# Kernel tuning notes

Hardware: AMD Instinct MI355X
Metric: run time of the kernel (lower is better)

Reference implementation:

```python
import jax, jax.numpy as jnp
import numpy as np

B, S, D, C = 4, 4096, 2048, 64  # batch, seq, d_model, num_channels (sqrt(4096)=64)
TEMP = 1.0
LN_EPS = 1e-5
AGG_EPS = 1e-8


def _layer_norm(x, g, b):
    m = x.mean(-1, keepdims=True)
    v = ((x - m) ** 2).mean(-1, keepdims=True)
    return (x - m) / jnp.sqrt(v + LN_EPS) * g + b


def setup_inputs() -> dict:
    key = jax.random.key(0)
    ks = jax.random.split(key, 8)
    s = 1.0 / np.sqrt(D)
    return {
        "x": jax.random.normal(ks[0], (B, S, D), jnp.float32),
        "attention_mask": jnp.ones((B, S), jnp.float32),
        "ln_gamma": jnp.ones((D,), jnp.float32),
        "ln_beta": jnp.zeros((D,), jnp.float32),
        "Wq": jax.random.normal(ks[1], (D, D), jnp.float32) * s,
        "Wk": jax.random.normal(ks[2], (D, D), jnp.float32) * s,
        "Wv": jax.random.normal(ks[3], (D, D), jnp.float32) * s,
        "Wr": jax.random.normal(ks[4], (C, D), jnp.float32) * s,
        "br": jnp.zeros((C,), jnp.float32),
        "Wa": jax.random.normal(ks[5], (D, D), jnp.float32) * s,
        "ba": jnp.zeros((D,), jnp.float32),
        "Wout": jax.random.normal(ks[6], (D, D), jnp.float32) * s,
        "bout": jnp.zeros((D,), jnp.float32),
    }


def reference(x, attention_mask, ln_gamma, ln_beta, Wq, Wk, Wv, Wr, br, Wa, ba, Wout, bout):
    residual = x
    h = _layer_norm(x, ln_gamma, ln_beta)
    q = h @ Wq.T  # [B,S,D]
    k = h @ Wk.T
    v = h @ Wv.T
    m = attention_mask[..., None]
    q = q * m
    k = k * m
    v = v * m

    # --- dynamic router: logits -> softmax, top-1 channel id + gathered weight ---
    routing_input = q + 0.1 * k
    probs = jax.nn.softmax((routing_input @ Wr.T + br) / TEMP, axis=-1)  # [B,S,C]
    channel_ids = jnp.argmax(probs, axis=-1)  # [B,S] int
    w = jnp.take_along_axis(probs, channel_ids[..., None], axis=-1)  # [B,S,1] top-1 weight

    # --- learnable channel aggregator: scatter-reduce tokens -> channels ---
    onehot = jax.nn.one_hot(channel_ids, C, dtype=v.dtype)  # [B,S,C]
    dispatch = onehot * w  # weighted dispatch mask
    ch_sum = jnp.einsum('bsc,bsd->bcd', dispatch, v)  # [B,C,D]
    ch_den = dispatch.sum(axis=1)  # [B,C]
    ch_mean = ch_sum / (ch_den[..., None] + AGG_EPS)
    ch_out = ch_mean @ Wa.T + ba  # learnable channel transform [B,C,D]
    # gather channel summary back to each token, weighted by routing weight
    aggregated = jnp.einsum('bsc,bcd->bsd', onehot, ch_out) * w  # [B,S,D]

    # --- regularization term ---
    q_norm = jnp.linalg.norm(q, axis=-1, keepdims=True)
    k_norm = jnp.linalg.norm(k, axis=-1, keepdims=True)
    reg = 0.001 * (q_norm + k_norm).mean()

    output = aggregated @ Wout.T + bout
    output = output + reg  # broadcast scalar reg_term
    output = output + residual
    return output
```

## Files before the change

kernel.cpp:

```cpp
#include <hip/hip_runtime.h>
#include <hip/hip_bf16.h>

typedef unsigned short u16;
typedef __bf16 bf16x8 __attribute__((ext_vector_type(8)));
typedef float  f32x4  __attribute__((ext_vector_type(4)));

#define B_   4
#define S_   4096
#define D_   2048
#define C_   64
#define T_   (B_*S_)
#define NALL 6144
#define NCH  16

__device__ __forceinline__ u16 f2bf(float f) {
  union { float f; unsigned u; } c; c.f = f;
  unsigned r = c.u + 0x7FFFu + ((c.u >> 16) & 1u);
  return (u16)(r >> 16);
}
__device__ __forceinline__ float bf2f(u16 u) {
  union { float f; unsigned u; } c; c.u = ((unsigned)u) << 16;
  return c.f;
}

__device__ __forceinline__ void gload16(const u16* g, u16* l) {
  __builtin_amdgcn_global_load_lds(
      (__attribute__((address_space(1))) void*)(void*)g,
      (__attribute__((address_space(3))) void*)l, 16, 0, 0);
}

#define BAR()  { __builtin_amdgcn_s_barrier(); __builtin_amdgcn_sched_barrier(0); }
#define VMW(N) { asm volatile("s_waitcnt vmcnt(" #N ")" ::: "memory"); __builtin_amdgcn_sched_barrier(0); }

template<int REGB, int TYPE>
__device__ __forceinline__ void stage_ht(const u16* __restrict__ Mat, char* lds,
                                         int bufbyte, int kelem, int wid, int lane)
{
#pragma unroll
  for (int j = 0; j < 2; ++j) {
    int sr;
    if (TYPE == 0)      sr = (j ?  64 :   0) + wid * 8;
    else if (TYPE == 1) sr = (j ? 192 : 128) + wid * 8;
    else if (TYPE == 2) sr = (j ? 128 :   0) + wid * 8;
    else                sr = (j ? 192 :  64) + wid * 8;
    int r  = sr + (lane >> 3);
    int kc = (lane & 7) ^ (lane >> 3);
    const u16* src = Mat + (size_t)r * 2048 + kelem + kc * 8;
    u16* dst = (u16*)(lds + bufbyte + REGB * 32768 + sr * 128 + lane * 16);
    gload16(src, dst);
  }
}

__global__ __launch_bounds__(512, 2)
void qkv8(const u16* __restrict__ A, const u16* __restrict__ BT,
          const float* __restrict__ mask,
          float* __restrict__ qn2, float* __restrict__ kn2,
          u16* __restrict__ vout)
{
  extern __shared__ char lds[];
  const int tid = threadIdx.x;
  const int wid = tid >> 6, lane = tid & 63;
  const int wm = wid >> 2, wn = wid & 3;
  const int lcol = lane & 15, lhi = lane >> 4, lc7 = lane & 7;
  const int bm = blockIdx.x, bn = blockIdx.y;

  const u16* Ab_ = A  + (size_t)bm * 256 * 2048;
  const u16* Bb_ = BT + (size_t)bn * 256 * 2048;

  f32x4 acc[8][4] = {};
  bf16x8 afr[4][2], bfr[4][2];

#define LDA_(f_, s_) (*(const bf16x8*)(lds + cbyte + ((wm*128 + (f_)*16 + lcol) * 128) + (((lhi + (s_)*4) ^ lc7) << 4)))
#define LDB_(g_, s_) (*(const bf16x8*)(lds + cbyte + 32768 + ((wn*64 + (g_)*16 + lcol) * 128) + (((lhi + (s_)*4) ^ lc7) << 4)))

  stage_ht<1, 0>(Bb_, lds, 0, 0, wid, lane);
  stage_ht<1, 1>(Bb_, lds, 0, 0, wid, lane);
  stage_ht<0, 2>(Ab_, lds, 0, 0, wid, lane);
  stage_ht<0, 3>(Ab_, lds, 0, 0, wid, lane);
  VMW(2); BAR();

#pragma unroll 2
  for (int kt = 0; kt < 32; ++kt) {
    const int cbyte = (kt & 1) * 65536;
    const int nbyte = cbyte ^ 65536;
    const int kel = ((kt + 1) & 31) * 64;

#pragma unroll
    for (int g = 0; g < 4; ++g)
#pragma unroll
      for (int s = 0; s < 2; ++s) bfr[g][s] = LDB_(g, s);
#pragma unroll
    for (int f = 0; f < 4; ++f)
#pragma unroll
      for (int s = 0; s < 2; ++s) afr[f][s] = LDA_(f, s);
    stage_ht<1, 0>(Bb_, lds, nbyte, kel, wid, lane);
    BAR();
    __builtin_amdgcn_s_setprio(1);
#pragma unroll
    for (int f = 0; f < 4; ++f)
#pragma unroll
      for (int g = 0; g < 2; ++g)
#pragma unroll
        for (int s = 0; s < 2; ++s)
          acc[f][g] = __builtin_amdgcn_mfma_f32_16x16x32_bf16(afr[f][s], bfr[g][s], acc[f][g], 0, 0, 0);
    __builtin_amdgcn_s_setprio(0);
    BAR();

    stage_ht<1, 1>(Bb_, lds, nbyte, kel, wid, lane);
    BAR();
    __builtin_amdgcn_s_setprio(1);
#pragma unroll
    for (int f = 0; f < 4; ++f)
#pragma unroll
      for (int g = 2; g < 4; ++g)
#pragma unroll
        for (int s = 0; s < 2; ++s)
          acc[f][g] = __builtin_amdgcn_mfma_f32_16x16x32_bf16(afr[f][s], bfr[g][s], acc[f][g], 0, 0, 0);
    __builtin_amdgcn_s_setprio(0);
    VMW(4); BAR();

#pragma unroll
    for (int f = 0; f < 4; ++f)
#pragma unroll
      for (int s = 0; s < 2; ++s) afr[f][s] = LDA_(f + 4, s);
    stage_ht<0, 2>(Ab_, lds, nbyte, kel, wid, lane);
    BAR();
    __builtin_amdgcn_s_setprio(1);
#pragma unroll
    for (int f = 0; f < 4; ++f)
#pragma unroll
      for (int g = 0; g < 2; ++g)
#pragma unroll
        for (int s = 0; s < 2; ++s)
          acc[f + 4][g] = __builtin_amdgcn_mfma_f32_16x16x32_bf16(afr[f][s], bfr[g][s], acc[f + 4][g], 0, 0, 0);
    __builtin_amdgcn_s_setprio(0);
    BAR();

    stage_ht<0, 3>(Ab_, lds, nbyte, kel, wid, lane);
    BAR();
    __builtin_amdgcn_s_setprio(1);
#pragma unroll
    for (int f = 0; f < 4; ++f)
#pragma unroll
      for (int g = 2; g < 4; ++g)
#pragma unroll
        for (int s = 0; s < 2; ++s)
          acc[f + 4][g] = __builtin_amdgcn_mfma_f32_16x16x32_bf16(afr[f][s], bfr[g][s], acc[f + 4][g], 0, 0, 0);
    __builtin_amdgcn_s_setprio(0);
    VMW(2); BAR();
  }
#undef LDA_
#undef LDB_

  const int region = bn >> 3;
  const int grow0 = bm * 256 + wm * 128;
  if (region < 2) {
    float* dst = region ? kn2 : qn2;
#pragma unroll
    for (int f = 0; f < 8; ++f)
#pragma unroll
      for (int i = 0; i < 4; ++i) {
        int row = grow0 + f * 16 + lhi * 4 + i;
        float mv = mask[row];
        float ss = 0.f;
#pragma unroll
        for (int g = 0; g < 4; ++g) { float v = acc[f][g][i] * mv; ss += v * v; }
#pragma unroll
        for (int d = 1; d < 16; d <<= 1) ss += __shfl_xor(ss, d);
        if (lcol == 0) atomicAdd(dst + row, ss);
      }
  } else {
    const int gcol0 = (bn - 16) * 256 + wn * 64 + lcol;
#pragma unroll
    for (int f = 0; f < 8; ++f)
#pragma unroll
      for (int i = 0; i < 4; ++i) {
        int row = grow0 + f * 16 + lhi * 4 + i;
        float mv = mask[row];
#pragma unroll
        for (int g = 0; g < 4; ++g)
          vout[(size_t)row * D_ + gcol0 + g * 16] = f2bf(acc[f][g][i] * mv);
      }
  }
}

template<int EPI>
__global__ __launch_bounds__(256)
void gemm_bt(const u16* __restrict__ A, const u16* __restrict__ BT, int K,
             u16* __restrict__ uout, float* __restrict__ fout,
             const float* __restrict__ bias)
{
  __shared__ u16 lA[128 * 32];
  __shared__ u16 lB[128 * 32];
  const int bm = blockIdx.x, bn = blockIdx.y;
  const int tid = threadIdx.x;
  const int wid = tid >> 6, lane = tid & 63;
  const int wm = wid >> 1, wn = wid & 1;
  const int lcol = lane & 15, khalf = lane >> 4;
  const int csw = khalf ^ ((lcol >> 1) & 3);
  const int kb = csw * 8;

  f32x4 acc[4][4] = {};

  const u16* Ab = A + (size_t)bm * 128 * K;
  const u16* Bb = BT + (size_t)bn * 128 * K;
  const int arow = wm * 64 + lcol;
  const int brow = wn * 64 + lcol;

  for (int kt = 0; kt < K; kt += 32) {
#pragma unroll
    for (int i = 0; i < 2; ++i) {
      int idx = tid + i * 256;
      int r = idx >> 2;
      int kc = (idx & 3) ^ ((r >> 1) & 3);
      int ko = kc << 3;
      gload16(Ab + (size_t)r * K + kt + ko, &lA[idx * 8]);
      gload16(Bb + (size_t)r * K + kt + ko, &lB[idx * 8]);
    }
    __syncthreads();
    bf16x8 av[4], bv[4];
#pragma unroll
    for (int f = 0; f < 4; ++f) {
      av[f] = *(const bf16x8*)&lA[(arow + f * 16) * 32 + kb];
      bv[f] = *(const bf16x8*)&lB[(brow + f * 16) * 32 + kb];
    }
#pragma unroll
    for (int m = 0; m < 4; ++m)
#pragma unroll
      for (int n = 0; n < 4; ++n)
        acc[m][n] = __builtin_amdgcn_mfma_f32_16x16x32_bf16(av[m], bv[n], acc[m][n], 0, 0, 0);
    __syncthreads();
  }

  const int r0 = bm * 128 + wm * 64;
  const int c0 = bn * 128 + wn * 64;
  const int lrow = khalf * 4;

  if constexpr (EPI == 2) {
#pragma unroll
    for (int fm = 0; fm < 4; ++fm)
#pragma unroll
      for (int i = 0; i < 4; ++i) {
        int row = r0 + fm * 16 + lrow + i;
#pragma unroll
        for (int fn = 0; fn < 4; ++fn) {
          int col = c0 + fn * 16 + lcol;
          uout[(size_t)row * D_ + col] = f2bf(acc[fm][fn][i] + bias[col]);
        }
      }
  } else {
#pragma unroll
    for (int fm = 0; fm < 4; ++fm)
#pragma unroll
      for (int i = 0; i < 4; ++i) {
        int row = r0 + fm * 16 + lrow + i;
#pragma unroll
        for (int fn = 0; fn < 4; ++fn) {
          int col = c0 + fn * 16 + lcol;
          fout[(size_t)row * D_ + col] = acc[fm][fn][i];
        }
      }
  }
}

__global__ __launch_bounds__(256)
void gemm4_bt(const u16* __restrict__ Ah, const u16* __restrict__ Al,
              const u16* __restrict__ Bh, const u16* __restrict__ Bl,
              int K, int rlim, float* __restrict__ out, int ldo)
{
  __shared__ u16 lAh[128 * 32];
  __shared__ u16 lAl[128 * 32];
  __shared__ u16 lBh[64 * 32];
  __shared__ u16 lBl[64 * 32];
  const int bm = blockIdx.x, bn = blockIdx.y;
  const int tid = threadIdx.x;
  const int wid = tid >> 6, lane = tid & 63;
  const int lcol = lane & 15, khalf = lane >> 4;
  const int csw = khalf ^ ((lcol >> 1) & 3);
  const int kb = csw * 8;

  f32x4 acc[2][4] = {};

  const u16* Abh = Ah + (size_t)bm * 128 * K;
  const u16* Abl = Al + (size_t)bm * 128 * K;
  const u16* Bbh = Bh + (size_t)bn * 64 * K;
  const u16* Bbl = Bl + (size_t)bn * 64 * K;
  const int arow = wid * 32 + lcol;

  for (int kt = 0; kt < K; kt += 32) {
#pragma unroll
    for (int i = 0; i < 2; ++i) {
      int idx = tid + i * 256;
      int r = idx >> 2;
      int kc = (idx & 3) ^ ((r >> 1) & 3);
      int ko = kc << 3;
      gload16(Abh + (size_t)r * K + kt + ko, &lAh[idx * 8]);
      gload16(Abl + (size_t)r * K + kt + ko, &lAl[idx * 8]);
    }
    {
      int r = tid >> 2;
      int kc = (tid & 3) ^ ((r >> 1) & 3);
      int ko = kc << 3;
      gload16(Bbh + (size_t)r * K + kt + ko, &lBh[tid * 8]);
      gload16(Bbl + (size_t)r * K + kt + ko, &lBl[tid * 8]);
    }
    __syncthreads();
    bf16x8 ah[2], al[2], bh[4], bl[4];
#pragma unroll
    for (int f = 0; f < 2; ++f) {
      ah[f] = *(const bf16x8*)&lAh[(arow + f * 16) * 32 + kb];
      al[f] = *(const bf16x8*)&lAl[(arow + f * 16) * 32 + kb];
    }
#pragma unroll
    for (int f = 0; f < 4; ++f) {
      bh[f] = *(const bf16x8*)&lBh[(f * 16 + lcol) * 32 + kb];
      bl[f] = *(const bf16x8*)&lBl[(f * 16 + lcol) * 32 + kb];
    }
#pragma unroll
    for (int m = 0; m < 2; ++m)
#pragma unroll
      for (int n = 0; n < 4; ++n) {
        acc[m][n] = __builtin_amdgcn_mfma_f32_16x16x32_bf16(ah[m], bh[n], acc[m][n], 0, 0, 0);
        acc[m][n] = __builtin_amdgcn_mfma_f32_16x16x32_bf16(ah[m], bl[n], acc[m][n], 0, 0, 0);
        acc[m][n] = __builtin_amdgcn_mfma_f32_16x16x32_bf16(al[m], bh[n], acc[m][n], 0, 0, 0);
        acc[m][n] = __builtin_amdgcn_mfma_f32_16x16x32_bf16(al[m], bl[n], acc[m][n], 0, 0, 0);
      }
    __syncthreads();
  }

  const int r0 = bm * 128 + wid * 32;
#pragma unroll
  for (int fm = 0; fm < 2; ++fm)
#pragma unroll
    for (int i = 0; i < 4; ++i) {
      int row = r0 + fm * 16 + khalf * 4 + i;
      if (row < rlim) {
#pragma unroll
        for (int fn = 0; fn < 4; ++fn) {
          int col = bn * 64 + fn * 16 + lcol;
          out[(size_t)row * ldo + col] = acc[fm][fn][i];
        }
      }
    }
}

__global__ __launch_bounds__(256)
void ln_kernel(const float* __restrict__ x, const float* __restrict__ g,
               const float* __restrict__ be, u16* __restrict__ h, u16* __restrict__ hl)
{
  const int row = blockIdx.x, tid = threadIdx.x;
  const int wid = tid >> 6, lane = tid & 63;
  const float* xr = x + (size_t)row * D_;
  float4 a = *(const float4*)(xr + tid * 4);
  float4 b = *(const float4*)(xr + 1024 + tid * 4);
  float s = a.x + a.y + a.z + a.w + b.x + b.y + b.z + b.w;
  float q = a.x * a.x + a.y * a.y + a.z * a.z + a.w * a.w +
            b.x * b.x + b.y * b.y + b.z * b.z + b.w * b.w;
#pragma unroll
  for (int d = 1; d < 64; d <<= 1) { s += __shfl_xor(s, d); q += __shfl_xor(q, d); }
  __shared__ float ls[4], lq[4];
  if (lane == 0) { ls[wid] = s; lq[wid] = q; }
  __syncthreads();
  s = ls[0] + ls[1] + ls[2] + ls[3];
  q = lq[0] + lq[1] + lq[2] + lq[3];
  const float mean = s * (1.0f / D_);
  const float var = q * (1.0f / D_) - mean * mean;
  const float rstd = rsqrtf(var + 1e-5f);

#pragma unroll
  for (int half = 0; half < 2; ++half) {
    int base = half * 1024 + tid * 4;
    float4 xv = half ? b : a;
    float4 gv = *(const float4*)(g + base);
    float4 bv = *(const float4*)(be + base);
    float v0 = (xv.x - mean) * rstd * gv.x + bv.x;
    float v1 = (xv.y - mean) * rstd * gv.y + bv.y;
    float v2 = (xv.z - mean) * rstd * gv.z + bv.z;
    float v3 = (xv.w - mean) * rstd * gv.w + bv.w;
    ushort4 oh, ol;
    oh.x = f2bf(v0); ol.x = f2bf(v0 - bf2f(oh.x));
    oh.y = f2bf(v1); ol.y = f2bf(v1 - bf2f(oh.y));
    oh.z = f2bf(v2); ol.z = f2bf(v2 - bf2f(oh.z));
    oh.w = f2bf(v3); ol.w = f2bf(v3 - bf2f(oh.w));
    *(ushort4*)(h  + (size_t)row * D_ + base) = oh;
    *(ushort4*)(hl + (size_t)row * D_ + base) = ol;
  }
}

__global__ __launch_bounds__(256)
void castf2b(const float* __restrict__ in, u16* __restrict__ out, int n)
{
  int i = (blockIdx.x * 256 + threadIdx.x) * 4;
  if (i >= n) return;
  float4 v = *(const float4*)(in + i);
  ushort4 o; o.x = f2bf(v.x); o.y = f2bf(v.y); o.z = f2bf(v.z); o.w = f2bf(v.w);
  *(ushort4*)(out + i) = o;
}

__global__ __launch_bounds__(256)
void splitf(const float* __restrict__ in, u16* __restrict__ hi, u16* __restrict__ lo, int n)
{
  int i = (blockIdx.x * 256 + threadIdx.x) * 4;
  if (i >= n) return;
  float4 v = *(const float4*)(in + i);
  ushort4 h, l;
  h.x = f2bf(v.x); l.x = f2bf(v.x - bf2f(h.x));
  h.y = f2bf(v.y); l.y = f2bf(v.y - bf2f(h.y));
  h.z = f2bf(v.z); l.z = f2bf(v.z - bf2f(h.z));
  h.w = f2bf(v.w); l.w = f2bf(v.w - bf2f(h.w));
  *(ushort4*)(hi + i) = h;
  *(ushort4*)(lo + i) = l;
}

__global__ __launch_bounds__(256)
void wqk_t(const float* __restrict__ Wq, const float* __restrict__ Wk,
           u16* __restrict__ Th, u16* __restrict__ Tl)
{
  __shared__ float t[32][33];
  const int bx = blockIdx.x * 32, by = blockIdx.y * 32;
  const int tx = threadIdx.x & 31, ty = threadIdx.x >> 5;
#pragma unroll
  for (int j = 0; j < 32; j += 8) {
    int aa = by + ty + j, ee = bx + tx;
    t[ty + j][tx] = Wq[(size_t)aa * D_ + ee] + 0.1f * Wk[(size_t)aa * D_ + ee];
  }
  __syncthreads();
#pragma unroll
  for (int j = 0; j < 32; j += 8) {
    int ee = bx + ty + j, aa = by + tx;
    float v = t[tx][ty + j];
    u16 h = f2bf(v);
    Th[(size_t)ee * D_ + aa] = h;
    Tl[(size_t)ee * D_ + aa] = f2bf(v - bf2f(h));
  }
}

__global__ __launch_bounds__(256)
void reg_reduce(const float* __restrict__ qn2, const float* __restrict__ kn2,
                float* __restrict__ racc)
{
  int i = blockIdx.x * 256 + threadIdx.x;
  int lane = threadIdx.x & 63, wid = threadIdx.x >> 6;
  float v = sqrtf(qn2[i]) + sqrtf(kn2[i]);
#pragma unroll
  for (int d = 1; d < 64; d <<= 1) v += __shfl_xor(v, d);
  __shared__ float lsum[4];
  if (lane == 0) lsum[wid] = v;
  __syncthreads();
  if (threadIdx.x == 0) atomicAdd(racc, lsum[0] + lsum[1] + lsum[2] + lsum[3]);
}

__global__ __launch_bounds__(256)
void router_kernel(const float* __restrict__ logits, const float* __restrict__ br,
                   int* __restrict__ cid, float* __restrict__ wt, float* __restrict__ chden)
{
  const int tid = threadIdx.x, wid = tid >> 6, lane = tid & 63;
  const int t = blockIdx.x * 4 + wid;
  float l = logits[(size_t)t * C_ + lane] + br[lane];
  float mx = l;
#pragma unroll
  for (int d = 1; d < 64; d <<= 1) mx = fmaxf(mx, __shfl_xor(mx, d));
  float e = __expf(l - mx);
  float s = e;
#pragma unroll
  for (int d = 1; d < 64; d <<= 1) s += __shfl_xor(s, d);
  unsigned long long ball = __ballot(l == mx);
  if (lane == 0) {
    int cstar = __ffsll(ball) - 1;
    float ww = 1.0f / s;
    cid[t] = cstar;
    wt[t] = ww;
    atomicAdd(&chden[(t >> 12) * C_ + cstar], ww);
  }
}

__global__ __launch_bounds__(256)
void scatter_kernel(const u16* __restrict__ v, const int* __restrict__ cid,
                    const float* __restrict__ w, float* __restrict__ partial)
{
  __shared__ float acc[C_ * 256];
  const int b = blockIdx.x, dt = blockIdx.y, st = blockIdx.z;
  const int tid = threadIdx.x;
  for (int i = tid; i < C_ * 256; i += 256) acc[i] = 0.f;
  __syncthreads();
  const int d = dt * 256 + tid;
  const int tbase = b * S_ + st * (S_ / NCH);
  for (int s = 0; s < S_ / NCH; ++s) {
    int t = tbase + s;
    int c = cid[t];
    float ww = w[t];
    acc[c * 256 + tid] += ww * bf2f(v[(size_t)t * D_ + d]);
  }
  __syncthreads();
  float* pb = partial + ((size_t)(b * NCH + st) * C_) * D_ + dt * 256;
  for (int i = tid; i < C_ * 256; i += 256) {
    int c = i >> 8, dd = i & 255;
    pb[(size_t)c * D_ + dd] = acc[i];
  }
}

__global__ __launch_bounds__(256)
void chmean_kernel(const float* __restrict__ partial, const float* __restrict__ chden,
                   u16* __restrict__ chmean)
{
  int idx = blockIdx.x * 256 + threadIdx.x;
  int d = idx & 2047, c = (idx >> 11) & 63, b = idx >> 17;
  float ssum = 0.f;
#pragma unroll
  for (int st = 0; st < NCH; ++st)
    ssum += partial[((size_t)(b * NCH + st) * C_ + c) * D_ + d];
  float den = chden[b * C_ + c];
  chmean[idx] = f2bf(ssum / (den + 1e-8f));
}

__global__ __launch_bounds__(256)
void finalize_kernel(const float* __restrict__ x, const float* __restrict__ bout,
                     const float* __restrict__ chproj, const int* __restrict__ cid,
                     const float* __restrict__ wt, const float* __restrict__ racc,
                     float* __restrict__ out)
{
  const int row = blockIdx.x, tid = threadIdx.x;
  const int b = row >> 12;
  const int c = cid[row];
  const float ww = wt[row];
  const float reg = racc[0] * (0.001f / (float)T_);
  const float* cp = chproj + (size_t)(b * C_ + c) * D_;
  const float* xr = x + (size_t)row * D_;
  float* orow = out + (size_t)row * D_;
#pragma unroll
  for (int base = 0; base < D_; base += 1024) {
    int d = base + tid * 4;
    float4 xv = *(const float4*)(xr + d);
    float4 cv = *(const float4*)(cp + d);
    float4 bv = *(const float4*)(bout + d);
    float4 o;
    o.x = ww * cv.x + bv.x + reg + xv.x;
    o.y = ww * cv.y + bv.y + reg + xv.y;
    o.z = ww * cv.z + bv.z + reg + xv.z;
    o.w = ww * cv.w + bv.w + reg + xv.w;
    *(float4*)(orow + d) = o;
  }
}

extern "C" void kernel_launch(void* const* d_in, const int* in_sizes, int n_in,
                              void* d_out, int out_size, void* d_ws, size_t ws_size,
                              hipStream_t stream)
{
  const float* x     = (const float*)d_in[0];
  const float* mask  = (const float*)d_in[1];
  const float* gamma = (const float*)d_in[2];
  const float* beta  = (const float*)d_in[3];
  const float* Wq    = (const float*)d_in[4];
  const float* Wk    = (const float*)d_in[5];
  const float* Wv    = (const float*)d_in[6];
  const float* Wr    = (const float*)d_in[7];
  const float* br    = (const float*)d_in[8];
  const float* Wa    = (const float*)d_in[9];
  const float* ba    = (const float*)d_in[10];
  const float* Wout  = (const float*)d_in[11];
  const float* bout  = (const float*)d_in[12];
  float* out = (float*)d_out;

  char* p = (char*)d_ws;
  size_t off = 0;
  auto take = [&](size_t bytes) -> void* {
    void* r = p + off;
    off = (off + bytes + 255) & ~(size_t)255;
    return r;
  };

  u16*   Wall   = (u16*)take((size_t)NALL * D_ * 2);
  u16*   WrPh   = (u16*)take((size_t)128 * D_ * 2);
  u16*   WrPl   = (u16*)take((size_t)128 * D_ * 2);
  u16*   Wqkh   = (u16*)take((size_t)D_ * D_ * 2);
  u16*   Wqkl   = (u16*)take((size_t)D_ * D_ * 2);
  u16*   WaB    = (u16*)take((size_t)D_ * D_ * 2);
  u16*   WoutB  = (u16*)take((size_t)D_ * D_ * 2);
  u16*   hbuf   = (u16*)take((size_t)T_ * D_ * 2);
  u16*   hlbuf  = (u16*)take((size_t)T_ * D_ * 2);
  u16*   vbuf   = (u16*)take((size_t)T_ * D_ * 2);
  float* Mf     = (float*)take((size_t)C_ * D_ * 4);
  u16*   Mh     = (u16*)take((size_t)C_ * D_ * 2);
  u16*   Ml     = (u16*)take((size_t)C_ * D_ * 2);
  float* logits = (float*)take((size_t)T_ * C_ * 4);
  float* partial= (float*)take((size_t)B_ * NCH * C_ * D_ * 4);
  float* chproj = (float*)take((size_t)B_ * C_ * D_ * 4);
  u16*   chmean = (u16*)take((size_t)B_ * C_ * D_ * 2);
  u16*   choutb = (u16*)take((size_t)B_ * C_ * D_ * 2);
  int*   cid    = (int*)take((size_t)T_ * 4);
  float* wt     = (float*)take((size_t)T_ * 4);
  char*  zbeg   = p + off;
  float* qn2    = (float*)take((size_t)T_ * 4);
  float* kn2    = (float*)take((size_t)T_ * 4);
  float* chden  = (float*)take((size_t)B_ * C_ * 4);
  float* racc   = (float*)take(256);
  size_t zlen   = (size_t)((p + off) - zbeg);

  hipMemsetAsync(zbeg, 0, zlen, stream);
  hipMemsetAsync(WrPh + (size_t)C_ * D_, 0, (size_t)C_ * D_ * 2, stream);
  hipMemsetAsync(WrPl + (size_t)C_ * D_, 0, (size_t)C_ * D_ * 2, stream);

  const int cb = 256;
  castf2b<<<dim3((D_ * D_) / 1024), cb, 0, stream>>>(Wq, Wall, D_ * D_);
  castf2b<<<dim3((D_ * D_) / 1024), cb, 0, stream>>>(Wk, Wall + (size_t)D_ * D_, D_ * D_);
  castf2b<<<dim3((D_ * D_) / 1024), cb, 0, stream>>>(Wv, Wall + (size_t)2 * D_ * D_, D_ * D_);
  castf2b<<<dim3((D_ * D_) / 1024), cb, 0, stream>>>(Wa, WaB, D_ * D_);
  castf2b<<<dim3((D_ * D_) / 1024), cb, 0, stream>>>(Wout, WoutB, D_ * D_);
  splitf<<<dim3((C_ * D_) / 1024), cb, 0, stream>>>(Wr, WrPh, WrPl, C_ * D_);
  wqk_t<<<dim3(64, 64), cb, 0, stream>>>(Wq, Wk, Wqkh, Wqkl);
  ln_kernel<<<dim3(T_), cb, 0, stream>>>(x, gamma, beta, hbuf, hlbuf);

  gemm4_bt<<<dim3(1, D_ / 64), cb, 0, stream>>>(WrPh, WrPl, Wqkh, Wqkl, D_, C_, Mf, D_);
  splitf<<<dim3((C_ * D_) / 1024), cb, 0, stream>>>(Mf, Mh, Ml, C_ * D_);
  gemm4_bt<<<dim3(T_ / 128, 1), cb, 0, stream>>>(hbuf, hlbuf, Mh, Ml, D_, T_, logits, C_);

  hipFuncSetAttribute((const void*)qkv8, hipFuncAttributeMaxDynamicSharedMemorySize, 131072);
  qkv8<<<dim3(T_ / 256, NALL / 256), 512, 131072, stream>>>(hbuf, Wall, mask, qn2, kn2, vbuf);

  reg_reduce<<<dim3(T_ / 256), cb, 0, stream>>>(qn2, kn2, racc);
  router_kernel<<<dim3(T_ / 4), cb, 0, stream>>>(logits, br, cid, wt, chden);
  scatter_kernel<<<dim3(B_, D_ / 256, NCH), cb, 0, stream>>>(vbuf, cid, wt, partial);
  chmean_kernel<<<dim3((B_ * C_ * D_) / 256), cb, 0, stream>>>(partial, chden, chmean);
  gemm_bt<2><<<dim3(2, 16), cb, 0, stream>>>(chmean, WaB, D_, choutb, nullptr, ba);
  gemm_bt<3><<<dim3(2, 16), cb, 0, stream>>>(choutb, WoutB, D_, nullptr, chproj, nullptr);
  finalize_kernel<<<dim3(T_), cb, 0, stream>>>(x, bout, chproj, cid, wt, racc, out);
}
```

Before: 1.078 ms.

## Restructure QKV GEMM main loop, swizzle tile order, and fuse prep launches

The QKV GEMM main loop now issues all four next-tile global loads at once and interleaves LDS fragment reads with MFMA quadrants using register double-buffering, so there are fewer barriers per iteration. It also remaps the flat block index so consecutive blocks share weight tiles in L2. On the host side, five cast launches, a split launch and three memsets become one prep kernel, zeroing moves into the layernorm kernel, and the reg reduction is folded into the router. Waiting on vmcnt(0) each iteration may reduce how well loads overlap with compute, and the register-held fragments raise register pressure.

```diff
diff --git a/kernel.cpp b/kernel.cpp
--- a/kernel.cpp
+++ b/kernel.cpp
@@ -12,6 +12,8 @@
 #define T_   (B_*S_)
 #define NALL 6144
 #define NCH  16
+#define DD   (D_*D_)
+#define CD   (C_*D_)
 
 __device__ __forceinline__ u16 f2bf(float f) {
   union { float f; unsigned u; } c; c.f = f;
@@ -30,7 +32,7 @@
 }
 
 #define BAR()  { __builtin_amdgcn_s_barrier(); __builtin_amdgcn_sched_barrier(0); }
-#define VMW(N) { asm volatile("s_waitcnt vmcnt(" #N ")" ::: "memory"); __builtin_amdgcn_sched_barrier(0); }
+#define VMW0() { asm volatile("s_waitcnt vmcnt(0)" ::: "memory"); __builtin_amdgcn_sched_barrier(0); }
 
 template<int REGB, int TYPE>
 __device__ __forceinline__ void stage_ht(const u16* __restrict__ Mat, char* lds,
@@ -62,22 +64,34 @@
   const int wid = tid >> 6, lane = tid & 63;
   const int wm = wid >> 2, wn = wid & 3;
   const int lcol = lane & 15, lhi = lane >> 4, lc7 = lane & 7;
-  const int bm = blockIdx.x, bn = blockIdx.y;
+
+  const int flat = blockIdx.x;
+  const int swz = (flat & 7) * 192 + (flat >> 3);
+  const int bm = swz & 63;
+  const int bn = swz >> 6;
 
   const u16* Ab_ = A  + (size_t)bm * 256 * 2048;
   const u16* Bb_ = BT + (size_t)bn * 256 * 2048;
 
   f32x4 acc[8][4] = {};
-  bf16x8 afr[4][2], bfr[4][2];
-
-#define LDA_(f_, s_) (*(const bf16x8*)(lds + cbyte + ((wm*128 + (f_)*16 + lcol) * 128) + (((lhi + (s_)*4) ^ lc7) << 4)))
-#define LDB_(g_, s_) (*(const bf16x8*)(lds + cbyte + 32768 + ((wn*64 + (g_)*16 + lcol) * 128) + (((lhi + (s_)*4) ^ lc7) << 4)))
+  bf16x8 aLo[4][2], aHi[4][2], bP[2][2], bHi[2][2];
+
+#define LDA_(bb_, f_, s_) (*(const bf16x8*)(lds + (bb_) + ((wm*128 + (f_)*16 + lcol) * 128) + (((lhi + (s_)*4) ^ lc7) << 4)))
+#define LDB_(bb_, g_, s_) (*(const bf16x8*)(lds + (bb_) + 32768 + ((wn*64 + (g_)*16 + lcol) * 128) + (((lhi + (s_)*4) ^ lc7) << 4)))
 
   stage_ht<1, 0>(Bb_, lds, 0, 0, wid, lane);
   stage_ht<1, 1>(Bb_, lds, 0, 0, wid, lane);
   stage_ht<0, 2>(Ab_, lds, 0, 0, wid, lane);
   stage_ht<0, 3>(Ab_, lds, 0, 0, wid, lane);
-  VMW(2); BAR();
+  VMW0(); BAR();
+#pragma unroll
+  for (int f = 0; f < 4; ++f)
+#pragma unroll
+    for (int s = 0; s < 2; ++s) aLo[f][s] = LDA_(0, f, s);
+#pragma unroll
+  for (int g = 0; g < 2; ++g)
+#pragma unroll
+    for (int s = 0; s < 2; ++s) bP[g][s] = LDB_(0, g, s);
 
 #pragma unroll 2
   for (int kt = 0; kt < 32; ++kt) {
@@ -86,68 +100,71 @@
     const int kel = ((kt + 1) & 31) * 64;
 
 #pragma unroll
-    for (int g = 0; g < 4; ++g)
-#pragma unroll
-      for (int s = 0; s < 2; ++s) bfr[g][s] = LDB_(g, s);
-#pragma unroll
-    for (int f = 0; f < 4; ++f)
-#pragma unroll
-      for (int s = 0; s < 2; ++s) afr[f][s] = LDA_(f, s);
+    for (int g = 0; g < 2; ++g)
+#pragma unroll
+      for (int s = 0; s < 2; ++s) bHi[g][s] = LDB_(cbyte, g + 2, s);
     stage_ht<1, 0>(Bb_, lds, nbyte, kel, wid, lane);
-    BAR();
-    __builtin_amdgcn_s_setprio(1);
-#pragma unroll
-    for (int f = 0; f < 4; ++f)
-#pragma unroll
-      for (int g = 0; g < 2; ++g)
-#pragma unroll
-        for (int s = 0; s < 2; ++s)
-          acc[f][g] = __builtin_amdgcn_mfma_f32_16x16x32_bf16(afr[f][s], bfr[g][s], acc[f][g], 0, 0, 0);
-    __builtin_amdgcn_s_setprio(0);
-    BAR();
-
     stage_ht<1, 1>(Bb_, lds, nbyte, kel, wid, lane);
-    BAR();
-    __builtin_amdgcn_s_setprio(1);
-#pragma unroll
-    for (int f = 0; f < 4; ++f)
-#pragma unroll
-      for (int g = 2; g < 4; ++g)
-#pragma unroll
-        for (int s = 0; s < 2; ++s)
-          acc[f][g] = __builtin_amdgcn_mfma_f32_16x16x32_bf16(afr[f][s], bfr[g][s], acc[f][g], 0, 0, 0);
-    __builtin_amdgcn_s_setprio(0);
-    VMW(4); BAR();
-
-#pragma unroll
-    for (int f = 0; f < 4; ++f)
-#pragma unroll
-      for (int s = 0; s < 2; ++s) afr[f][s] = LDA_(f + 4, s);
     stage_ht<0, 2>(Ab_, lds, nbyte, kel, wid, lane);
-    BAR();
-    __builtin_amdgcn_s_setprio(1);
-#pragma unroll
-    for (int f = 0; f < 4; ++f)
-#pragma unroll
-      for (int g = 0; g < 2; ++g)
-#pragma unroll
-        for (int s = 0; s < 2; ++s)
-          acc[f + 4][g] = __builtin_amdgcn_mfma_f32_16x16x32_bf16(afr[f][s], bfr[g][s], acc[f + 4][g], 0, 0, 0);
-    __builtin_amdgcn_s_setprio(0);
-    BAR();
-
     stage_ht<0, 3>(Ab_, lds, nbyte, kel, wid, lane);
     BAR();
     __builtin_amdgcn_s_setprio(1);
 #pragma unroll
     for (int f = 0; f < 4; ++f)
 #pragma unroll
-      for (int g = 2; g < 4; ++g)
+      for (int g = 0; g < 2; ++g)
 #pragma unroll
         for (int s = 0; s < 2; ++s)
-          acc[f + 4][g] = __builtin_amdgcn_mfma_f32_16x16x32_bf16(afr[f][s], bfr[g][s], acc[f + 4][g], 0, 0, 0);
+          acc[f][g] = __builtin_amdgcn_mfma_f32_16x16x32_bf16(aLo[f][s], bP[g][s], acc[f][g], 0, 0, 0);
     __builtin_amdgcn_s_setprio(0);
-    VMW(2); BAR();
+    BAR();
+
+#pragma unroll
+    for (int f = 0; f < 4; ++f)
+#pragma unroll
+      for (int s = 0; s < 2; ++s) aHi[f][s] = LDA_(cbyte, f + 4, s);
+    BAR();
+    __builtin_amdgcn_s_setprio(1);
+#pragma unroll
+    for (int f = 0; f < 4; ++f)
+#pragma unroll
+      for (int g = 0; g < 2; ++g)
+#pragma unroll
+        for (int s = 0; s < 2; ++s)
+          acc[f][g + 2] = __builtin_amdgcn_mfma_f32_16x16x32_bf16(aLo[f][s], bHi[g][s], acc[f][g + 2], 0, 0, 0);
+    __builtin_amdgcn_s_setprio(0);
+    BAR();
+
+    VMW0(); BAR();
+#pragma unroll
+    for (int f = 0; f < 4; ++f)
+#pragma unroll
+      for (int s = 0; s < 2; ++s) aLo[f][s] = LDA_(nbyte, f, s);
+    __builtin_amdgcn_s_setprio(1);
+#pragma unroll
+    for (int f = 0; f < 4; ++f)
+#pragma unroll
+      for (int g = 0; g < 2; ++g)
+#pragma unroll
+        for (int s = 0; s < 2; ++s)
+          acc[f + 4][g] = __builtin_amdgcn_mfma_f32_16x16x32_bf16(aHi[f][s], bP[g][s], acc[f + 4][g], 0, 0, 0);
+    __builtin_amdgcn_s_setprio(0);
+    BAR();
+
+#pragma unroll
+    for (int g = 0; g < 2; ++g)
+#pragma unroll
+      for (int s = 0; s < 2; ++s) bP[g][s] = LDB_(nbyte, g, s);
+    __builtin_amdgcn_s_setprio(1);
+#pragma unroll
+    for (int f = 0; f < 4; ++f)
+#pragma unroll
+      for (int g = 0; g < 2; ++g)
+#pragma unroll
+        for (int s = 0; s < 2; ++s)
+          acc[f + 4][g + 2] = __builtin_amdgcn_mfma_f32_16x16x32_bf16(aHi[f][s], bHi[g][s], acc[f + 4][g + 2], 0, 0, 0);
+    __builtin_amdgcn_s_setprio(0);
+    BAR();
   }
 #undef LDA_
 #undef LDB_
@@ -346,10 +363,17 @@
 
 __global__ __launch_bounds__(256)
 void ln_kernel(const float* __restrict__ x, const float* __restrict__ g,
-               const float* __restrict__ be, u16* __restrict__ h, u16* __restrict__ hl)
+               const float* __restrict__ be, u16* __restrict__ h, u16* __restrict__ hl,
+               float* __restrict__ qn2, float* __restrict__ kn2,
+               float* __restrict__ chden, float* __restrict__ racc)
 {
   const int row = blockIdx.x, tid = threadIdx.x;
   const int wid = tid >> 6, lane = tid & 63;
+  if (tid == 0) {
+    qn2[row] = 0.f; kn2[row] = 0.f;
+    if (row < B_ * C_) chden[row] = 0.f;
+    if (row == 0) racc[0] = 0.f;
+  }
   const float* xr = x + (size_t)row * D_;
   float4 a = *(const float4*)(xr + tid * 4);
   float4 b = *(const float4*)(xr + 1024 + tid * 4);
@@ -388,13 +412,39 @@
 }
 
 __global__ __launch_bounds__(256)
-void castf2b(const float* __restrict__ in, u16* __restrict__ out, int n)
+void prep(const float* __restrict__ Wq, const float* __restrict__ Wk,
+          const float* __restrict__ Wv, const float* __restrict__ Wa,
+          const float* __restrict__ Wout, const float* __restrict__ Wr,
+          u16* __restrict__ Wall, u16* __restrict__ WaB, u16* __restrict__ WoutB,
+          u16* __restrict__ WrPh, u16* __restrict__ WrPl)
 {
   int i = (blockIdx.x * 256 + threadIdx.x) * 4;
-  if (i >= n) return;
-  float4 v = *(const float4*)(in + i);
+  const float* src; u16* dst; int j;
+  if (i < 3 * DD)      { src = (i < DD) ? Wq : (i < 2 * DD) ? Wk : Wv;
+                         j = i % DD; dst = Wall + (i / DD) * (size_t)DD; }
+  else if (i < 4 * DD) { src = Wa;   j = i - 3 * DD; dst = WaB; }
+  else if (i < 5 * DD) { src = Wout; j = i - 4 * DD; dst = WoutB; }
+  else if (i < 5 * DD + CD) {
+    j = i - 5 * DD;
+    float4 v = *(const float4*)(Wr + j);
+    ushort4 h, l;
+    h.x = f2bf(v.x); l.x = f2bf(v.x - bf2f(h.x));
+    h.y = f2bf(v.y); l.y = f2bf(v.y - bf2f(h.y));
+    h.z = f2bf(v.z); l.z = f2bf(v.z - bf2f(h.z));
+    h.w = f2bf(v.w); l.w = f2bf(v.w - bf2f(h.w));
+    *(ushort4*)(WrPh + j) = h;
+    *(ushort4*)(WrPl + j) = l;
+    return;
+  } else {
+    j = i - (5 * DD + CD);
+    ushort4 z = {0, 0, 0, 0};
+    *(ushort4*)(WrPh + CD + j) = z;
+    *(ushort4*)(WrPl + CD + j) = z;
+    return;
+  }
+  float4 v = *(const float4*)(src + j);
   ushort4 o; o.x = f2bf(v.x); o.y = f2bf(v.y); o.z = f2bf(v.z); o.w = f2bf(v.w);
-  *(ushort4*)(out + i) = o;
+  *(ushort4*)(dst + j) = o;
 }
 
 __global__ __launch_bounds__(256)
@@ -436,23 +486,10 @@
 }
 
 __global__ __launch_bounds__(256)
-void reg_reduce(const float* __restrict__ qn2, const float* __restrict__ kn2,
-                float* __restrict__ racc)
-{
-  int i = blockIdx.x * 256 + threadIdx.x;
-  int lane = threadIdx.x & 63, wid = threadIdx.x >> 6;
-  float v = sqrtf(qn2[i]) + sqrtf(kn2[i]);
-#pragma unroll
-  for (int d = 1; d < 64; d <<= 1) v += __shfl_xor(v, d);
-  __shared__ float lsum[4];
-  if (lane == 0) lsum[wid] = v;
-  __syncthreads();
-  if (threadIdx.x == 0) atomicAdd(racc, lsum[0] + lsum[1] + lsum[2] + lsum[3]);
-}
-
-__global__ __launch_bounds__(256)
 void router_kernel(const float* __restrict__ logits, const float* __restrict__ br,
-                   int* __restrict__ cid, float* __restrict__ wt, float* __restrict__ chden)
+                   const float* __restrict__ qn2, const float* __restrict__ kn2,
+                   int* __restrict__ cid, float* __restrict__ wt,
+                   float* __restrict__ chden, float* __restrict__ racc)
 {
   const int tid = threadIdx.x, wid = tid >> 6, lane = tid & 63;
   const int t = blockIdx.x * 4 + wid;
@@ -465,13 +502,17 @@
 #pragma unroll
   for (int d = 1; d < 64; d <<= 1) s += __shfl_xor(s, d);
   unsigned long long ball = __ballot(l == mx);
+  __shared__ float lsum[4];
   if (lane == 0) {
     int cstar = __ffsll(ball) - 1;
     float ww = 1.0f / s;
     cid[t] = cstar;
     wt[t] = ww;
     atomicAdd(&chden[(t >> 12) * C_ + cstar], ww);
-  }
+    lsum[wid] = sqrtf(qn2[t]) + sqrtf(kn2[t]);
+  }
+  __syncthreads();
+  if (tid == 0) atomicAdd(racc, lsum[0] + lsum[1] + lsum[2] + lsum[3]);
 }
 
 __global__ __launch_bounds__(256)
@@ -589,36 +630,25 @@
   u16*   choutb = (u16*)take((size_t)B_ * C_ * D_ * 2);
   int*   cid    = (int*)take((size_t)T_ * 4);
   float* wt     = (float*)take((size_t)T_ * 4);
-  char*  zbeg   = p + off;
   float* qn2    = (float*)take((size_t)T_ * 4);
   float* kn2    = (float*)take((size_t)T_ * 4);
   float* chden  = (float*)take((size_t)B_ * C_ * 4);
   float* racc   = (float*)take(256);
-  size_t zlen   = (size_t)((p + off) - zbeg);
-
-  hipMemsetAsync(zbeg, 0, zlen, stream);
-  hipMemsetAsync(WrPh + (size_t)C_ * D_, 0, (size_t)C_ * D_ * 2, stream);
-  hipMemsetAsync(WrPl + (size_t)C_ * D_, 0, (size_t)C_ * D_ * 2, stream);
 
   const int cb = 256;
-  castf2b<<<dim3((D_ * D_) / 1024), cb, 0, stream>>>(Wq, Wall, D_ * D_);
-  castf2b<<<dim3((D_ * D_) / 1024), cb, 0, stream>>>(Wk, Wall + (size_t)D_ * D_, D_ * D_);
-  castf2b<<<dim3((D_ * D_) / 1024), cb, 0, stream>>>(Wv, Wall + (size_t)2 * D_ * D_, D_ * D_);
-  castf2b<<<dim3((D_ * D_) / 1024), cb, 0, stream>>>(Wa, WaB, D_ * D_);
-  castf2b<<<dim3((D_ * D_) / 1024), cb, 0, stream>>>(Wout, WoutB, D_ * D_);
-  splitf<<<dim3((C_ * D_) / 1024), cb, 0, stream>>>(Wr, WrPh, WrPl, C_ * D_);
+  prep<<<dim3((5 * DD + 2 * CD) / 1024), cb, 0, stream>>>(Wq, Wk, Wv, Wa, Wout, Wr,
+                                                          Wall, WaB, WoutB, WrPh, WrPl);
   wqk_t<<<dim3(64, 64), cb, 0, stream>>>(Wq, Wk, Wqkh, Wqkl);
-  ln_kernel<<<dim3(T_), cb, 0, stream>>>(x, gamma, beta, hbuf, hlbuf);
+  ln_kernel<<<dim3(T_), cb, 0, stream>>>(x, gamma, beta, hbuf, hlbuf, qn2, kn2, chden, racc);
 
   gemm4_bt<<<dim3(1, D_ / 64), cb, 0, stream>>>(WrPh, WrPl, Wqkh, Wqkl, D_, C_, Mf, D_);
   splitf<<<dim3((C_ * D_) / 1024), cb, 0, stream>>>(Mf, Mh, Ml, C_ * D_);
   gemm4_bt<<<dim3(T_ / 128, 1), cb, 0, stream>>>(hbuf, hlbuf, Mh, Ml, D_, T_, logits, C_);
 
   hipFuncSetAttribute((const void*)qkv8, hipFuncAttributeMaxDynamicSharedMemorySize, 131072);
-  qkv8<<<dim3(T_ / 256, NALL / 256), 512, 131072, stream>>>(hbuf, Wall, mask, qn2, kn2, vbuf);
-
-  reg_reduce<<<dim3(T_ / 256), cb, 0, stream>>>(qn2, kn2, racc);
-  router_kernel<<<dim3(T_ / 4), cb, 0, stream>>>(logits, br, cid, wt, chden);
+  qkv8<<<dim3((T_ / 256) * (NALL / 256)), 512, 131072, stream>>>(hbuf, Wall, mask, qn2, kn2, vbuf);
+
+  router_kernel<<<dim3(T_ / 4), cb, 0, stream>>>(logits, br, qn2, kn2, cid, wt, chden, racc);
   scatter_kernel<<<dim3(B_, D_ / 256, NCH), cb, 0, stream>>>(vbuf, cid, wt, partial);
   chmean_kernel<<<dim3((B_ * C_ * D_) / 256), cb, 0, stream>>>(partial, chden, chmean);
   gemm_bt<2><<<dim3(2, 16), cb, 0, stream>>>(chmean, WaB, D_, choutb, nullptr, ba);
```

Measured after the change: 1.566 ms. +45.3%, slower.
